# Optimization experiments

Measured on AMD Instinct MI355X. Metric: run time of the kernel, lower is better.

## Reference

```python
import jax, jax.numpy as jnp
import numpy as np

B, C, H, W = 8, 256, 64, 64
CR = C // 8  # reduced channels = 32


def setup_inputs() -> dict:
    key = jax.random.key(0)
    k1, k2, k3, k4 = jax.random.split(key, 4)
    x = jax.random.normal(k1, (B, C, H, W), dtype=jnp.float32)
    # 1x1 conv weights (bias=False) are plain channel matmuls; scale like kaiming (~1/sqrt(fan_in))
    Wt = jax.random.normal(k2, (3 * CR, C), dtype=jnp.float32) * (1.0 / np.sqrt(C))
    Wo = jax.random.normal(k3, (C, CR), dtype=jnp.float32) * (1.0 / np.sqrt(CR))
    scale = jax.random.normal(k4, (1,), dtype=jnp.float32)
    return {"x": x, "Wt": Wt, "Wo": Wo, "scale": scale}


def reference(x, Wt, Wo, scale):
    b, c, h, w = x.shape
    n = h * w
    # 1x1 conv QKV projection: [B, 3*Cr, H, W]
    t = jnp.einsum('oc,bchw->bohw', Wt, x)
    cr = t.shape[1] // 3
    key = t[:, :cr].reshape(b, cr, n)          # [B, Cr, N]
    query = t[:, cr:2 * cr].reshape(b, cr, n)  # [B, Cr, N]
    value = t[:, 2 * cr:].reshape(b, cr, n)    # [B, Cr, N]
    # scores[b, i, j] = sum_c key[b,c,i] * query[b,c,j]  (key^T @ query)
    scores = jnp.einsum('bci,bcj->bij', key, query)  # [B, N, N]
    # torch Softmax(dim=1): normalize over the key axis i
    weights = jax.nn.softmax(scores, axis=1)
    # output[b, c, j] = sum_i value[b,c,i] * weights[b,i,j]
    out = jnp.einsum('bci,bij->bcj', value, weights)  # [B, Cr, N]
    out = out.reshape(b, cr, h, w)
    out = jnp.einsum('oc,bchw->bohw', Wo, out)  # 1x1 conv back to C channels
    return scale[0] * out + x
```

## Files before the change

### kernel.cpp

```cpp
#include <hip/hip_runtime.h>
#include <math.h>

#define B_ 8
#define C_ 256
#define CR_ 32
#define N_ 4096
#define NH_ 4

typedef __attribute__((ext_vector_type(8))) short bf16x8;
typedef __attribute__((ext_vector_type(4))) short bf16x4;
typedef __attribute__((ext_vector_type(4))) float f32x4;
typedef __attribute__((ext_vector_type(16))) float f32x16;
typedef __attribute__((ext_vector_type(2))) unsigned uint32x2;

#if defined(__has_builtin)
#if __has_builtin(__builtin_amdgcn_permlane32_swap)
#define HAVE_PLSWAP 1
#endif
#endif

__device__ inline short f2bf(float f) {
  union { float f; unsigned u; } v; v.f = f;
  unsigned r = v.u + 0x7FFFu + ((v.u >> 16) & 1u);
  return (short)(r >> 16);
}
__device__ inline float bf2f(short h) {
  union { unsigned u; float f; } v; v.u = ((unsigned)(unsigned short)h) << 16;
  return v.f;
}
__device__ inline short f2bf_r(float f) {
  return (short)((__float_as_uint(f) + 0x8000u) >> 16);
}

__global__ __launch_bounds__(256) void prep_weights(const float* __restrict__ Wt,
                                                    const float* __restrict__ Wo,
                                                    const float* __restrict__ scale,
                                                    short* __restrict__ WtHi,
                                                    short* __restrict__ WtLo,
                                                    short* __restrict__ WoB) {
  const int blk = blockIdx.x, tid = threadIdx.x;
  if (blk < 96) {
    float v = Wt[blk * C_ + tid];
    if (blk >= 32 && blk < 64) v *= 1.44269504f;
    const short h = f2bf(v);
    WtHi[blk * C_ + tid] = h;
    WtLo[blk * C_ + tid] = f2bf(v - bf2f(h));
  } else {
    const int idx = (blk - 96) * 256 + tid;
    WoB[idx] = f2bf(Wo[idx] * scale[0]);
  }
}

__global__ __launch_bounds__(256) void qkv_mfma(const float* __restrict__ x,
                                                const short* __restrict__ WtHi,
                                                const short* __restrict__ WtLo,
                                                short* __restrict__ t_tr,
                                                short* __restrict__ Vg) {
  const int b = blockIdx.y;
  const int tid = threadIdx.x;
  const int wave = tid >> 6, lane = tid & 63;
  const int col = lane & 15, quad = lane >> 4;
  const int n0 = (blockIdx.x * 4 + wave) * 16;

  const f32x4 z4 = {0.f, 0.f, 0.f, 0.f};
  f32x4 acc[6] = {z4, z4, z4, z4, z4, z4};

  const float* xb = x + (size_t)b * C_ * N_ + n0 + col;
  float xcur[8], xnxt[8];
#pragma unroll
  for (int j = 0; j < 8; ++j) xcur[j] = xb[(size_t)(quad * 8 + j) * N_];

#pragma unroll 2
  for (int c0 = 0; c0 < C_; c0 += 32) {
    if (c0 < C_ - 32) {
#pragma unroll
      for (int j = 0; j < 8; ++j)
        xnxt[j] = xb[(size_t)(c0 + 32 + quad * 8 + j) * N_];
    }
    bf16x8 xh, xl;
#pragma unroll
    for (int j = 0; j < 8; ++j) {
      const short h = (short)(__float_as_uint(xcur[j]) >> 16);
      xh[j] = h;
      xl[j] = f2bf_r(xcur[j] - bf2f(h));
    }
#pragma unroll
    for (int ot = 0; ot < 4; ++ot) {
      const int off = (ot * 16 + col) * C_ + c0 + quad * 8;
      const bf16x8 bh = *(const bf16x8*)(WtHi + off);
      const bf16x8 bl = *(const bf16x8*)(WtLo + off);
      acc[ot] = __builtin_amdgcn_mfma_f32_16x16x32_bf16(xh, bh, acc[ot], 0, 0, 0);
      acc[ot] = __builtin_amdgcn_mfma_f32_16x16x32_bf16(xl, bh, acc[ot], 0, 0, 0);
      acc[ot] = __builtin_amdgcn_mfma_f32_16x16x32_bf16(xh, bl, acc[ot], 0, 0, 0);
    }
#pragma unroll
    for (int ct = 0; ct < 2; ++ct) {
      const int off = ((64 + ct * 16) + col) * C_ + c0 + quad * 8;
      const bf16x8 ah = *(const bf16x8*)(WtHi + off);
      const bf16x8 al = *(const bf16x8*)(WtLo + off);
      acc[4 + ct] = __builtin_amdgcn_mfma_f32_16x16x32_bf16(ah, xh, acc[4 + ct], 0, 0, 0);
      acc[4 + ct] = __builtin_amdgcn_mfma_f32_16x16x32_bf16(ah, xl, acc[4 + ct], 0, 0, 0);
      acc[4 + ct] = __builtin_amdgcn_mfma_f32_16x16x32_bf16(al, xh, acc[4 + ct], 0, 0, 0);
    }
#pragma unroll
    for (int j = 0; j < 8; ++j) xcur[j] = xnxt[j];
  }
#pragma unroll
  for (int ot = 0; ot < 4; ++ot)
#pragma unroll
    for (int r = 0; r < 4; ++r)
      t_tr[((size_t)b * N_ + n0 + quad * 4 + r) * 64 + ot * 16 + col] =
          f2bf(acc[ot][r]);
#pragma unroll
  for (int ct = 0; ct < 2; ++ct)
#pragma unroll
    for (int r = 0; r < 4; ++r)
      Vg[(size_t)b * CR_ * N_ + (size_t)(ct * 16 + quad * 4 + r) * N_ + n0 + col] =
          f2bf(acc[4 + ct][r]);
}

__global__ __launch_bounds__(64, 4) void flash_attn(const short* __restrict__ t_tr,
                                                    const short* __restrict__ Vg,
                                                    short* __restrict__ OPart,
                                                    float* __restrict__ LPart) {
  const int b = blockIdx.z, hq = blockIdx.y;
  const int j0 = blockIdx.x * 32;
  const int lane = threadIdx.x;
  const int j32 = lane & 31, h32 = lane >> 5;
  const short* T = t_tr + (size_t)b * N_ * 64;
  const short* V = Vg + (size_t)b * CR_ * N_;

  const f32x16 z16 = {0.f};
  const short* Qrow = T + (size_t)(j0 + j32) * 64 + 32 + h32 * 8;
  const bf16x8 qf0 = *(const bf16x8*)(Qrow);
  const bf16x8 qf1 = *(const bf16x8*)(Qrow + 16);

  f32x16 acc = z16;
  float ps = 0.f;

  const int ibase = hq * 1024;

#pragma unroll 1
  for (int iter = 0; iter < 16; ++iter) {
    const int i0 = ibase + iter * 64;
#pragma unroll
    for (int it = 0; it < 2; ++it) {
      const int ioff = i0 + it * 32;
      const short* Trow = T + (size_t)(ioff + j32) * 64 + h32 * 8;
      const bf16x8 ka = *(const bf16x8*)(Trow);
      const bf16x8 kb = *(const bf16x8*)(Trow + 16);
      const short* Vrow = V + (size_t)j32 * N_ + ioff + h32 * 8;
      const bf16x8 va = *(const bf16x8*)(Vrow);
      const bf16x8 vb = *(const bf16x8*)(Vrow + 16);
      __builtin_amdgcn_s_setprio(1);
      f32x16 s = __builtin_amdgcn_mfma_f32_32x32x16_bf16(ka, qf0, z16, 0, 0, 0);
      s = __builtin_amdgcn_mfma_f32_32x32x16_bf16(kb, qf1, s, 0, 0, 0);
      __builtin_amdgcn_s_setprio(0);
      float p[16];
#pragma unroll
      for (int r = 0; r < 16; ++r) p[r] = __builtin_amdgcn_exp2f(s[r]);
      ps += (((p[0] + p[1]) + (p[2] + p[3])) + ((p[4] + p[5]) + (p[6] + p[7]))) +
            (((p[8] + p[9]) + (p[10] + p[11])) + ((p[12] + p[13]) + (p[14] + p[15])));
      unsigned d[8];
#pragma unroll
      for (int k = 0; k < 8; ++k) {
        const unsigned u0 = __float_as_uint(p[2 * k]) + 0x8000u;
        const unsigned u1 = __float_as_uint(p[2 * k + 1]) + 0x8000u;
        d[k] = __builtin_amdgcn_perm(u1, u0, 0x07060302u);
      }
      union { unsigned u[4]; bf16x8 v; } f0, f1;
#ifdef HAVE_PLSWAP
      {
        const uint32x2 r0 = __builtin_amdgcn_permlane32_swap(d[0], d[2], false, false);
        f0.u[0] = r0[0]; f0.u[2] = r0[1];
        const uint32x2 r1 = __builtin_amdgcn_permlane32_swap(d[1], d[3], false, false);
        f0.u[1] = r1[0]; f0.u[3] = r1[1];
        const uint32x2 r2 = __builtin_amdgcn_permlane32_swap(d[4], d[6], false, false);
        f1.u[0] = r2[0]; f1.u[2] = r2[1];
        const uint32x2 r3 = __builtin_amdgcn_permlane32_swap(d[5], d[7], false, false);
        f1.u[1] = r3[0]; f1.u[3] = r3[1];
      }
#else
      {
        unsigned xw[8];
#pragma unroll
        for (int k = 0; k < 8; ++k) xw[k] = __shfl_xor((int)d[k], 32);
        f0.u[0] = h32 ? xw[2] : d[0];
        f0.u[1] = h32 ? xw[3] : d[1];
        f0.u[2] = h32 ? d[2] : xw[0];
        f0.u[3] = h32 ? d[3] : xw[1];
        f1.u[0] = h32 ? xw[6] : d[4];
        f1.u[1] = h32 ? xw[7] : d[5];
        f1.u[2] = h32 ? d[6] : xw[4];
        f1.u[3] = h32 ? d[7] : xw[5];
      }
#endif
      __builtin_amdgcn_s_setprio(1);
      acc = __builtin_amdgcn_mfma_f32_32x32x16_bf16(va, f0.v, acc, 0, 0, 0);
      acc = __builtin_amdgcn_mfma_f32_32x32x16_bf16(vb, f1.v, acc, 0, 0, 0);
      __builtin_amdgcn_s_setprio(0);
    }
  }

  const size_t base = ((size_t)b * NH_ + hq) * N_;
  const float l = ps + __shfl_xor(ps, 32);
  const int jg = j0 + j32;
  if (h32 == 0) LPart[base + jg] = l;
  short* OP = OPart + (base + jg) * 32;
#pragma unroll
  for (int g = 0; g < 4; ++g) {
    bf16x4 o = {f2bf(acc[4 * g + 0]), f2bf(acc[4 * g + 1]),
                f2bf(acc[4 * g + 2]), f2bf(acc[4 * g + 3])};
    *(bf16x4*)(OP + 8 * g + 4 * h32) = o;
  }
}

__global__ __launch_bounds__(256) void out_proj(const short* __restrict__ OPart,
                                                const float* __restrict__ LPart,
                                                const short* __restrict__ WoB,
                                                const float* __restrict__ x,
                                                float* __restrict__ out) {
  const int b = blockIdx.z, chalf = blockIdx.y;
  const int tid = threadIdx.x;
  const int wave = tid >> 6, lane = tid & 63;
  const int col = lane & 15, quad = lane >> 4;
  const int jg = blockIdx.x * 64 + wave * 16 + col;
  const int n0 = blockIdx.x * 64 + wave * 16;

  float osum[8];
#pragma unroll
  for (int e = 0; e < 8; ++e) osum[e] = 0.f;
  float lsum = 0.f;
#pragma unroll
  for (int h = 0; h < NH_; ++h) {
    const size_t p = ((size_t)b * NH_ + h) * N_ + jg;
    const bf16x8 o = *(const bf16x8*)(OPart + p * 32 + quad * 8);
#pragma unroll
    for (int e = 0; e < 8; ++e) osum[e] += bf2f(o[e]);
    lsum += LPart[p];
  }
  const float linv = 1.f / lsum;
  bf16x8 bf;
#pragma unroll
  for (int e = 0; e < 8; ++e) bf[e] = f2bf(osum[e] * linv);

  const f32x4 z4 = {0.f, 0.f, 0.f, 0.f};
  const float* xb = x + (size_t)b * C_ * N_;
  float* ob = out + (size_t)b * C_ * N_;
#pragma unroll
  for (int ct = 0; ct < 8; ++ct) {
    const int ctg = chalf * 8 + ct;
    const bf16x8 af = *(const bf16x8*)(WoB + (ctg * 16 + col) * 32 + quad * 8);
    const f32x4 a = __builtin_amdgcn_mfma_f32_16x16x32_bf16(af, bf, z4, 0, 0, 0);
#pragma unroll
    for (int r = 0; r < 4; ++r) {
      const size_t idx = (size_t)(ctg * 16 + quad * 4 + r) * N_ + n0 + col;
      ob[idx] = a[r] + xb[idx];
    }
  }
}

extern "C" void kernel_launch(void* const* d_in, const int* in_sizes, int n_in,
                              void* d_out, int out_size, void* d_ws,
                              size_t ws_size, hipStream_t stream) {
  const float* x = (const float*)d_in[0];
  const float* Wt = (const float*)d_in[1];
  const float* Wo = (const float*)d_in[2];
  const float* scale = (const float*)d_in[3];
  float* out = (float*)d_out;

  short* OPart = (short*)d_ws;
  float* LPart = (float*)(OPart + (size_t)B_ * NH_ * N_ * 32);
  short* t_tr = (short*)(LPart + (size_t)B_ * NH_ * N_);
  short* Vg = t_tr + (size_t)B_ * N_ * 64;
  short* WtHi = Vg + (size_t)B_ * CR_ * N_;
  short* WtLo = WtHi + 96 * C_;
  short* WoB = WtLo + 96 * C_;

  prep_weights<<<dim3(128), 256, 0, stream>>>(Wt, Wo, scale, WtHi, WtLo, WoB);
  qkv_mfma<<<dim3(64, B_), 256, 0, stream>>>(x, WtHi, WtLo, t_tr, Vg);
  flash_attn<<<dim3(128, NH_, B_), 64, 0, stream>>>(t_tr, Vg, OPart, LPart);
  out_proj<<<dim3(64, 2, B_), 256, 0, stream>>>(OPart, LPart, WoB, x, out);
}
```

Before: 183.6 us.

## Store K/Q/V in MFMA fragment-native layout and prefetch next tile in attention

The QKV projection now writes K, Q and V into separate buffers laid out so each lane's MFMA operand fragment is one contiguous 16-byte chunk, with each 64-lane tile fully contiguous. The attention loop then reads fully coalesced 1KB blocks per fragment instead of strided row reads, and software-prefetches the next K/V tile into registers before computing the current one. This aims to cut memory transaction count and hide load latency. The cost is scattered stores in the projection kernel and extra live registers in attention.

New measurement: 152.3 us. 1.21x faster.

```diff
diff --git a/kernel.cpp b/kernel.cpp
--- a/kernel.cpp
+++ b/kernel.cpp
@@ -31,6 +31,7 @@
 __device__ inline short f2bf_r(float f) {
   return (short)((__float_as_uint(f) + 0x8000u) >> 16);
 }
+
 
 __global__ __launch_bounds__(256) void prep_weights(const float* __restrict__ Wt,
                                                     const float* __restrict__ Wo,
@@ -54,8 +55,9 @@
 __global__ __launch_bounds__(256) void qkv_mfma(const float* __restrict__ x,
                                                 const short* __restrict__ WtHi,
                                                 const short* __restrict__ WtLo,
-                                                short* __restrict__ t_tr,
-                                                short* __restrict__ Vg) {
+                                                short* __restrict__ Kf,
+                                                short* __restrict__ Qf,
+                                                short* __restrict__ Vf) {
   const int b = blockIdx.y;
   const int tid = threadIdx.x;
   const int wave = tid >> 6, lane = tid & 63;
@@ -105,106 +107,128 @@
 #pragma unroll
     for (int j = 0; j < 8; ++j) xcur[j] = xnxt[j];
   }
-#pragma unroll
-  for (int ot = 0; ot < 4; ++ot)
-#pragma unroll
-    for (int r = 0; r < 4; ++r)
-      t_tr[((size_t)b * N_ + n0 + quad * 4 + r) * 64 + ot * 16 + col] =
+
+#pragma unroll
+  for (int ot = 0; ot < 2; ++ot)
+#pragma unroll
+    for (int r = 0; r < 4; ++r) {
+      const int i = n0 + quad * 4 + r;
+      const int c = ot * 16 + col;
+      const int ln = (i & 31) | (((c >> 3) & 1) << 5);
+      Kf[(((size_t)(b * 128 + (i >> 5)) * 2 + (c >> 4)) * 64 + ln) * 8 + (c & 7)] =
           f2bf(acc[ot][r]);
+    }
+#pragma unroll
+  for (int ot = 2; ot < 4; ++ot)
+#pragma unroll
+    for (int r = 0; r < 4; ++r) {
+      const int j = n0 + quad * 4 + r;
+      const int c = (ot - 2) * 16 + col;
+      const int ln = (j & 31) | (((c >> 3) & 1) << 5);
+      Qf[(((size_t)(b * 128 + (j >> 5)) * 2 + (c >> 4)) * 64 + ln) * 8 + (c & 7)] =
+          f2bf(acc[ot][r]);
+    }
 #pragma unroll
   for (int ct = 0; ct < 2; ++ct)
 #pragma unroll
-    for (int r = 0; r < 4; ++r)
-      Vg[(size_t)b * CR_ * N_ + (size_t)(ct * 16 + quad * 4 + r) * N_ + n0 + col] =
+    for (int r = 0; r < 4; ++r) {
+      const int c = ct * 16 + quad * 4 + r;
+      const int n = n0 + col;
+      const int ln = c | (((n >> 3) & 1) << 5);
+      Vf[((size_t)(b * 256 + (n >> 4)) * 64 + ln) * 8 + (n & 7)] =
           f2bf(acc[4 + ct][r]);
-}
-
-__global__ __launch_bounds__(64, 4) void flash_attn(const short* __restrict__ t_tr,
-                                                    const short* __restrict__ Vg,
+    }
+}
+
+__global__ __launch_bounds__(64, 4) void flash_attn(const short* __restrict__ Kf,
+                                                    const short* __restrict__ Qf,
+                                                    const short* __restrict__ Vf,
                                                     short* __restrict__ OPart,
                                                     float* __restrict__ LPart) {
   const int b = blockIdx.z, hq = blockIdx.y;
-  const int j0 = blockIdx.x * 32;
+  const int jt = blockIdx.x;
   const int lane = threadIdx.x;
   const int j32 = lane & 31, h32 = lane >> 5;
-  const short* T = t_tr + (size_t)b * N_ * 64;
-  const short* V = Vg + (size_t)b * CR_ * N_;
 
   const f32x16 z16 = {0.f};
-  const short* Qrow = T + (size_t)(j0 + j32) * 64 + 32 + h32 * 8;
-  const bf16x8 qf0 = *(const bf16x8*)(Qrow);
-  const bf16x8 qf1 = *(const bf16x8*)(Qrow + 16);
+  const short* pQ = Qf + ((size_t)(b * 128 + jt) * 2) * 512 + lane * 8;
+  const bf16x8 qf0 = *(const bf16x8*)(pQ);
+  const bf16x8 qf1 = *(const bf16x8*)(pQ + 512);
+
+  const short* pK = Kf + ((size_t)(b * 128 + hq * 32) * 2) * 512 + lane * 8;
+  const short* pV = Vf + ((size_t)(b * 256 + hq * 64)) * 512 + lane * 8;
 
   f32x16 acc = z16;
   float ps = 0.f;
 
-  const int ibase = hq * 1024;
+  bf16x8 ka = *(const bf16x8*)(pK);
+  bf16x8 kb = *(const bf16x8*)(pK + 512);
+  bf16x8 va = *(const bf16x8*)(pV);
+  bf16x8 vb = *(const bf16x8*)(pV + 512);
 
 #pragma unroll 1
-  for (int iter = 0; iter < 16; ++iter) {
-    const int i0 = ibase + iter * 64;
-#pragma unroll
-    for (int it = 0; it < 2; ++it) {
-      const int ioff = i0 + it * 32;
-      const short* Trow = T + (size_t)(ioff + j32) * 64 + h32 * 8;
-      const bf16x8 ka = *(const bf16x8*)(Trow);
-      const bf16x8 kb = *(const bf16x8*)(Trow + 16);
-      const short* Vrow = V + (size_t)j32 * N_ + ioff + h32 * 8;
-      const bf16x8 va = *(const bf16x8*)(Vrow);
-      const bf16x8 vb = *(const bf16x8*)(Vrow + 16);
-      __builtin_amdgcn_s_setprio(1);
-      f32x16 s = __builtin_amdgcn_mfma_f32_32x32x16_bf16(ka, qf0, z16, 0, 0, 0);
-      s = __builtin_amdgcn_mfma_f32_32x32x16_bf16(kb, qf1, s, 0, 0, 0);
-      __builtin_amdgcn_s_setprio(0);
-      float p[16];
-#pragma unroll
-      for (int r = 0; r < 16; ++r) p[r] = __builtin_amdgcn_exp2f(s[r]);
-      ps += (((p[0] + p[1]) + (p[2] + p[3])) + ((p[4] + p[5]) + (p[6] + p[7]))) +
-            (((p[8] + p[9]) + (p[10] + p[11])) + ((p[12] + p[13]) + (p[14] + p[15])));
-      unsigned d[8];
-#pragma unroll
-      for (int k = 0; k < 8; ++k) {
-        const unsigned u0 = __float_as_uint(p[2 * k]) + 0x8000u;
-        const unsigned u1 = __float_as_uint(p[2 * k + 1]) + 0x8000u;
-        d[k] = __builtin_amdgcn_perm(u1, u0, 0x07060302u);
-      }
-      union { unsigned u[4]; bf16x8 v; } f0, f1;
+  for (int t = 0; t < 32; ++t) {
+    pK += 1024;
+    pV += 1024;
+    const bf16x8 kan = *(const bf16x8*)(pK);
+    const bf16x8 kbn = *(const bf16x8*)(pK + 512);
+    const bf16x8 van = *(const bf16x8*)(pV);
+    const bf16x8 vbn = *(const bf16x8*)(pV + 512);
+
+    __builtin_amdgcn_s_setprio(1);
+    f32x16 s = __builtin_amdgcn_mfma_f32_32x32x16_bf16(ka, qf0, z16, 0, 0, 0);
+    s = __builtin_amdgcn_mfma_f32_32x32x16_bf16(kb, qf1, s, 0, 0, 0);
+    __builtin_amdgcn_s_setprio(0);
+    float p[16];
+#pragma unroll
+    for (int r = 0; r < 16; ++r) p[r] = __builtin_amdgcn_exp2f(s[r]);
+    ps += (((p[0] + p[1]) + (p[2] + p[3])) + ((p[4] + p[5]) + (p[6] + p[7]))) +
+          (((p[8] + p[9]) + (p[10] + p[11])) + ((p[12] + p[13]) + (p[14] + p[15])));
+    unsigned d[8];
+#pragma unroll
+    for (int k = 0; k < 8; ++k) {
+      const unsigned u0 = __float_as_uint(p[2 * k]) + 0x8000u;
+      const unsigned u1 = __float_as_uint(p[2 * k + 1]) + 0x8000u;
+      d[k] = __builtin_amdgcn_perm(u1, u0, 0x07060302u);
+    }
+    union { unsigned u[4]; bf16x8 v; } f0, f1;
 #ifdef HAVE_PLSWAP
-      {
-        const uint32x2 r0 = __builtin_amdgcn_permlane32_swap(d[0], d[2], false, false);
-        f0.u[0] = r0[0]; f0.u[2] = r0[1];
-        const uint32x2 r1 = __builtin_amdgcn_permlane32_swap(d[1], d[3], false, false);
-        f0.u[1] = r1[0]; f0.u[3] = r1[1];
-        const uint32x2 r2 = __builtin_amdgcn_permlane32_swap(d[4], d[6], false, false);
-        f1.u[0] = r2[0]; f1.u[2] = r2[1];
-        const uint32x2 r3 = __builtin_amdgcn_permlane32_swap(d[5], d[7], false, false);
-        f1.u[1] = r3[0]; f1.u[3] = r3[1];
-      }
+    {
+      const uint32x2 r0 = __builtin_amdgcn_permlane32_swap(d[0], d[2], false, false);
+      f0.u[0] = r0[0]; f0.u[2] = r0[1];
+      const uint32x2 r1 = __builtin_amdgcn_permlane32_swap(d[1], d[3], false, false);
+      f0.u[1] = r1[0]; f0.u[3] = r1[1];
+      const uint32x2 r2 = __builtin_amdgcn_permlane32_swap(d[4], d[6], false, false);
+      f1.u[0] = r2[0]; f1.u[2] = r2[1];
+      const uint32x2 r3 = __builtin_amdgcn_permlane32_swap(d[5], d[7], false, false);
+      f1.u[1] = r3[0]; f1.u[3] = r3[1];
+    }
 #else
-      {
-        unsigned xw[8];
-#pragma unroll
-        for (int k = 0; k < 8; ++k) xw[k] = __shfl_xor((int)d[k], 32);
-        f0.u[0] = h32 ? xw[2] : d[0];
-        f0.u[1] = h32 ? xw[3] : d[1];
-        f0.u[2] = h32 ? d[2] : xw[0];
-        f0.u[3] = h32 ? d[3] : xw[1];
-        f1.u[0] = h32 ? xw[6] : d[4];
-        f1.u[1] = h32 ? xw[7] : d[5];
-        f1.u[2] = h32 ? d[6] : xw[4];
-        f1.u[3] = h32 ? d[7] : xw[5];
-      }
+    {
+      unsigned xw[8];
+#pragma unroll
+      for (int k = 0; k < 8; ++k) xw[k] = __shfl_xor((int)d[k], 32);
+      f0.u[0] = h32 ? xw[2] : d[0];
+      f0.u[1] = h32 ? xw[3] : d[1];
+      f0.u[2] = h32 ? d[2] : xw[0];
+      f0.u[3] = h32 ? d[3] : xw[1];
+      f1.u[0] = h32 ? xw[6] : d[4];
+      f1.u[1] = h32 ? xw[7] : d[5];
+      f1.u[2] = h32 ? d[6] : xw[4];
+      f1.u[3] = h32 ? d[7] : xw[5];
+    }
 #endif
-      __builtin_amdgcn_s_setprio(1);
-      acc = __builtin_amdgcn_mfma_f32_32x32x16_bf16(va, f0.v, acc, 0, 0, 0);
-      acc = __builtin_amdgcn_mfma_f32_32x32x16_bf16(vb, f1.v, acc, 0, 0, 0);
-      __builtin_amdgcn_s_setprio(0);
-    }
+    __builtin_amdgcn_s_setprio(1);
+    acc = __builtin_amdgcn_mfma_f32_32x32x16_bf16(va, f0.v, acc, 0, 0, 0);
+    acc = __builtin_amdgcn_mfma_f32_32x32x16_bf16(vb, f1.v, acc, 0, 0, 0);
+    __builtin_amdgcn_s_setprio(0);
+
+    ka = kan; kb = kbn; va = van; vb = vbn;
   }
 
   const size_t base = ((size_t)b * NH_ + hq) * N_;
   const float l = ps + __shfl_xor(ps, 32);
-  const int jg = j0 + j32;
+  const int jg = jt * 32 + j32;
   if (h32 == 0) LPart[base + jg] = l;
   short* OP = OPart + (base + jg) * 32;
 #pragma unroll
@@ -271,14 +295,15 @@
 
   short* OPart = (short*)d_ws;
   float* LPart = (float*)(OPart + (size_t)B_ * NH_ * N_ * 32);
-  short* t_tr = (short*)(LPart + (size_t)B_ * NH_ * N_);
-  short* Vg = t_tr + (size_t)B_ * N_ * 64;
-  short* WtHi = Vg + (size_t)B_ * CR_ * N_;
+  short* Kf = (short*)(LPart + (size_t)B_ * NH_ * N_);
+  short* Qf = Kf + (size_t)B_ * 128 * 1024;
+  short* Vf = Qf + (size_t)B_ * 128 * 1024;
+  short* WtHi = Vf + (size_t)B_ * 256 * 512;
   short* WtLo = WtHi + 96 * C_;
   short* WoB = WtLo + 96 * C_;
 
   prep_weights<<<dim3(128), 256, 0, stream>>>(Wt, Wo, scale, WtHi, WtLo, WoB);
-  qkv_mfma<<<dim3(64, B_), 256, 0, stream>>>(x, WtHi, WtLo, t_tr, Vg);
-  flash_attn<<<dim3(128, NH_, B_), 64, 0, stream>>>(t_tr, Vg, OPart, LPart);
+  qkv_mfma<<<dim3(64, B_), 256, 0, stream>>>(x, WtHi, WtLo, Kf, Qf, Vf);
+  flash_attn<<<dim3(128, NH_, B_), 64, 0, stream>>>(Kf, Qf, Vf, OPart, LPart);
   out_proj<<<dim3(64, 2, B_), 256, 0, stream>>>(OPart, LPart, WoB, x, out);
 }
```
